# Optimization experiments

Hardware: AMD Instinct MI355X
Metric: run time of the kernel (lower is better)

Reference implementation:

```python
import jax, jax.numpy as jnp
import numpy as np

N_NODES = 50000
N_EDGES = 600000
IN_CH = 128
HID = 128
OUT_CH = 1
N_GRAPHS = 64


def setup_inputs() -> dict:
    key = jax.random.key(0)
    ks = jax.random.split(key, 16)
    inp = {
        "x": jax.random.normal(ks[0], (N_NODES, IN_CH), dtype=jnp.float32),
        "edge_index": jax.random.randint(ks[1], (2, N_EDGES), 0, N_NODES, dtype=jnp.int64),
        "edge_weight": jax.random.uniform(ks[2], (N_EDGES,), dtype=jnp.float32),
        "batch": jnp.sort(jax.random.randint(ks[3], (N_NODES,), 0, N_GRAPHS, dtype=jnp.int64)),
    }
    # SAGEConv params: lin_l (neighbor-aggregate path, has bias) and lin_r (root path)
    dims = [(IN_CH, HID), (HID, HID), (HID, HID), (HID, HID)]
    for i, (din, dout) in enumerate(dims, start=1):
        s = 1.0 / np.sqrt(din)
        inp[f"Wl{i}"] = jax.random.uniform(ks[3 + 2 * i], (din, dout), minval=-s, maxval=s, dtype=jnp.float32)
        inp[f"Wr{i}"] = jax.random.uniform(ks[4 + 2 * i], (din, dout), minval=-s, maxval=s, dtype=jnp.float32)
        inp[f"b{i}"] = jnp.zeros((dout,), dtype=jnp.float32)
    s = 1.0 / np.sqrt(HID)
    inp["Wc"] = jax.random.uniform(ks[14], (HID, OUT_CH), minval=-s, maxval=s, dtype=jnp.float32)
    inp["bc"] = jnp.zeros((OUT_CH,), dtype=jnp.float32)
    return inp


def _sage_conv(x, src, dst, Wl, Wr, b):
    # mean aggregation of source-node features at each destination node
    msg = x[src]  # [E, d] gather
    agg = jax.ops.segment_sum(msg, dst, num_segments=N_NODES)
    cnt = jax.ops.segment_sum(jnp.ones((src.shape[0],), x.dtype), dst, num_segments=N_NODES)
    agg = agg / jnp.maximum(cnt, 1.0)[:, None]
    return agg @ Wl + b + x @ Wr


def reference(x, edge_index, edge_weight, batch,
              Wl1, Wr1, b1, Wl2, Wr2, b2, Wl3, Wr3, b3, Wl4, Wr4, b4, Wc, bc):
    src, dst = edge_index[0], edge_index[1]
    h = jax.nn.relu(_sage_conv(x, src, dst, Wl1, Wr1, b1))
    h = jax.nn.relu(_sage_conv(h, src, dst, Wl2, Wr2, b2))
    h = jax.nn.relu(_sage_conv(h, src, dst, Wl3, Wr3, b3))
    h = jax.nn.relu(_sage_conv(h, src, dst, Wl4, Wr4, b4))
    # global mean pool over graphs
    pooled = jax.ops.segment_sum(h, batch, num_segments=N_GRAPHS)
    gcnt = jax.ops.segment_sum(jnp.ones((N_NODES,), h.dtype), batch, num_segments=N_GRAPHS)
    pooled = pooled / jnp.maximum(gcnt, 1.0)[:, None]  # [G, HID]
    return jax.nn.sigmoid(pooled @ Wc + bc)  # [G, 1]
```

## Files before the change

### kernel.cpp

```cpp
#include <hip/hip_runtime.h>
#include <math.h>

#define NND 50000
#define LNP 50048
#define NED 600000
#define CD  128
#define NG  64
#define NBLK 196
#define GROWS 64

typedef short s8v  __attribute__((ext_vector_type(8)));
typedef float f4v  __attribute__((ext_vector_type(4)));
typedef float f2v  __attribute__((ext_vector_type(2)));
typedef unsigned short u16x4 __attribute__((ext_vector_type(4)));
typedef unsigned short u16x8 __attribute__((ext_vector_type(8)));

static __device__ __forceinline__ unsigned short f2bf(float f) {
  union { float f; unsigned u; } v; v.f = f;
  unsigned r = v.u + 0x7fffu + ((v.u >> 16) & 1u);
  return (unsigned short)(r >> 16);
}
static __device__ __forceinline__ float bf2f(unsigned short h) {
  union { unsigned u; float f; } v; v.u = ((unsigned)h) << 16; return v.f;
}
static __device__ __forceinline__ unsigned f2fp8x4(float a, float b, float c, float d) {
  int r = __builtin_amdgcn_cvt_pk_fp8_f32(a, b, 0, false);
  r = __builtin_amdgcn_cvt_pk_fp8_f32(c, d, r, true);
  return (unsigned)r;
}
static __device__ __forceinline__ void g2lds(const unsigned short* g, unsigned short* l) {
  __builtin_amdgcn_global_load_lds(
      (const __attribute__((address_space(1))) unsigned*)g,
      (__attribute__((address_space(3))) unsigned*)l, 16, 0, 0);
}

__global__ __launch_bounds__(256) void bsum_k(const int* __restrict__ cnt,
                                              int* __restrict__ bsum) {
  __shared__ int s[256];
  int i = blockIdx.x * 256 + threadIdx.x;
  s[threadIdx.x] = (i < NND) ? cnt[i] : 0;
  __syncthreads();
  for (int off = 128; off > 0; off >>= 1) {
    if (threadIdx.x < off) s[threadIdx.x] += s[threadIdx.x + off];
    __syncthreads();
  }
  if (threadIdx.x == 0) bsum[blockIdx.x] = s[0];
}

__global__ __launch_bounds__(256) void bscan_k(const int* __restrict__ bsum,
                                               int* __restrict__ boff,
                                               int* __restrict__ offs,
                                               const int* __restrict__ batch,
                                               int* __restrict__ gb) {
  __shared__ int s[256];
  int t = threadIdx.x;
  if (t <= NG) {
    int lo = 0, hi = NND;
    while (lo < hi) {
      int mid = (lo + hi) >> 1;
      if (batch[mid] < t) lo = mid + 1; else hi = mid;
    }
    gb[t] = lo;
  }
  s[t] = (t < NBLK) ? bsum[t] : 0;
  __syncthreads();
  for (int off = 1; off < 256; off <<= 1) {
    int v = (t >= off) ? s[t - off] : 0;
    __syncthreads();
    s[t] += v;
    __syncthreads();
  }
  if (t < NBLK) boff[t] = (t == 0) ? 0 : s[t - 1];
  if (t == NBLK - 1) offs[NND] = s[t];
}

__global__ __launch_bounds__(256) void escan_k(const int* __restrict__ cnt,
                                               const int* __restrict__ boff,
                                               int* __restrict__ offs,
                                               int* __restrict__ cur) {
  __shared__ int s[256];
  int i = blockIdx.x * 256 + threadIdx.x;
  int t = threadIdx.x;
  int v = (i < NND) ? cnt[i] : 0;
  s[t] = v;
  __syncthreads();
  for (int off = 1; off < 256; off <<= 1) {
    int u = (t >= off) ? s[t - off] : 0;
    __syncthreads();
    s[t] += u;
    __syncthreads();
  }
  if (i < NND) {
    int excl = s[t] - v + boff[blockIdx.x];
    offs[i] = excl;
    cur[i]  = excl;
  }
}

__global__ void fill_k(const int* __restrict__ src, const int* __restrict__ dst,
                       int* __restrict__ cur, int* __restrict__ csr) {
  int e = blockIdx.x * blockDim.x + threadIdx.x;
  if (e >= NED) return;
  int d = dst[e];
  int pos = atomicAdd(&cur[d], 1);
  csr[pos] = src[e];
}

struct WPtrs { const float* w[8]; unsigned short* wt[8]; };
__global__ void prep_k(const float* __restrict__ x, unsigned short* __restrict__ xb,
                       unsigned* __restrict__ x8, WPtrs p,
                       const int* __restrict__ dst, int* __restrict__ cnt) {
  int t = blockIdx.x * blockDim.x + threadIdx.x;
  if (t < NND * 32) {
    float4 v = reinterpret_cast<const float4*>(x)[t];
    u16x4 o;
    o.x = f2bf(v.x); o.y = f2bf(v.y); o.z = f2bf(v.z); o.w = f2bf(v.w);
    reinterpret_cast<u16x4*>(xb)[t] = o;
    x8[t] = f2fp8x4(v.x, v.y, v.z, v.w);
  } else {
    int u = t - NND * 32;
    if (u < 8 * CD * CD) {
      int m = u >> 14, r = u & (CD * CD - 1);
      int n = r >> 7, k = r & 127;
      p.wt[m][r] = f2bf(p.w[m][k * CD + n]);
    } else {
      int e = u - 8 * CD * CD;
      if (e < NED) atomicAdd(&cnt[dst[e]], 1);
    }
  }
}

__global__ __launch_bounds__(256, 4) void sage_k(
    const unsigned* __restrict__ xq, const unsigned short* __restrict__ xb,
    const int* __restrict__ csr, const int* __restrict__ offs,
    const unsigned short* __restrict__ WlT, const unsigned short* __restrict__ WrT,
    const float* __restrict__ bias, unsigned short* __restrict__ hb,
    unsigned char* __restrict__ h8) {
  __shared__ unsigned short abuf[GROWS * CD];
  __shared__ unsigned short xbuf[GROWS * CD];

  const int tid  = threadIdx.x;
  const int wave = tid >> 6;
  const int lane = tid & 63;
  const int quad = lane >> 4;
  const int l16  = lane & 15;
  const size_t rbase = (size_t)blockIdx.x * GROWS;

#pragma unroll
  for (int j = 0; j < 4; ++j) {
    const int s = j * 256 + tid;
    g2lds(xb + (rbase + (s >> 4)) * CD + (s & 15) * 8, &xbuf[(size_t)s * 8]);
  }

  s8v bL[2][4], bR[2][4];
#pragma unroll
  for (int nt = 0; nt < 2; ++nt) {
    const int n = wave * 32 + nt * 16 + l16;
#pragma unroll
    for (int kk = 0; kk < 4; ++kk) {
      size_t woff = (size_t)n * CD + kk * 32 + quad * 8;
      bL[nt][kk] = *reinterpret_cast<const s8v*>(WlT + woff);
      bR[nt][kk] = *reinterpret_cast<const s8v*>(WrT + woff);
    }
  }
  const float bv0 = bias[wave * 32 + l16];
  const float bv1 = bias[wave * 32 + 16 + l16];

  const int team = tid >> 4;
  const int tl   = tid & 15;
  const unsigned* base = xq + tl * 2;
  for (int i = 0; i < 4; ++i) {
    const int rl = team * 4 + i;
    const size_t row = rbase + rl;
    u16x8 o = {};
    if (row < NND) {
      const int e0 = offs[row], e1 = offs[row + 1];
      f2v a01 = {0.f, 0.f}, a23 = {0.f, 0.f}, a45 = {0.f, 0.f}, a67 = {0.f, 0.f};
      int e = e0;
      for (; e + 8 <= e1; e += 8) {
        int s[8];
#pragma unroll
        for (int j = 0; j < 8; ++j) s[j] = csr[e + j];
        uint2 v[8];
#pragma unroll
        for (int j = 0; j < 8; ++j)
          v[j] = *reinterpret_cast<const uint2*>(base + (size_t)s[j] * 32);
#pragma unroll
        for (int j = 0; j < 8; ++j) {
          a01 += __builtin_amdgcn_cvt_pk_f32_fp8(v[j].x, false);
          a23 += __builtin_amdgcn_cvt_pk_f32_fp8(v[j].x, true);
          a45 += __builtin_amdgcn_cvt_pk_f32_fp8(v[j].y, false);
          a67 += __builtin_amdgcn_cvt_pk_f32_fp8(v[j].y, true);
        }
      }
      for (; e + 4 <= e1; e += 4) {
        int s[4];
#pragma unroll
        for (int j = 0; j < 4; ++j) s[j] = csr[e + j];
        uint2 v[4];
#pragma unroll
        for (int j = 0; j < 4; ++j)
          v[j] = *reinterpret_cast<const uint2*>(base + (size_t)s[j] * 32);
#pragma unroll
        for (int j = 0; j < 4; ++j) {
          a01 += __builtin_amdgcn_cvt_pk_f32_fp8(v[j].x, false);
          a23 += __builtin_amdgcn_cvt_pk_f32_fp8(v[j].x, true);
          a45 += __builtin_amdgcn_cvt_pk_f32_fp8(v[j].y, false);
          a67 += __builtin_amdgcn_cvt_pk_f32_fp8(v[j].y, true);
        }
      }
      for (; e < e1; ++e) {
        uint2 v = *reinterpret_cast<const uint2*>(base + (size_t)csr[e] * 32);
        a01 += __builtin_amdgcn_cvt_pk_f32_fp8(v.x, false);
        a23 += __builtin_amdgcn_cvt_pk_f32_fp8(v.x, true);
        a45 += __builtin_amdgcn_cvt_pk_f32_fp8(v.y, false);
        a67 += __builtin_amdgcn_cvt_pk_f32_fp8(v.y, true);
      }
      const float invd = 1.0f / fmaxf((float)(e1 - e0), 1.0f);
      o[0] = f2bf(a01.x * invd); o[1] = f2bf(a01.y * invd);
      o[2] = f2bf(a23.x * invd); o[3] = f2bf(a23.y * invd);
      o[4] = f2bf(a45.x * invd); o[5] = f2bf(a45.y * invd);
      o[6] = f2bf(a67.x * invd); o[7] = f2bf(a67.y * invd);
    }
    *reinterpret_cast<u16x8*>(abuf + rl * CD + tl * 8) = o;
  }

  __syncthreads();

#pragma unroll
  for (int rt = 0; rt < GROWS / 16; ++rt) {
    const unsigned short* arow = abuf + (rt * 16 + l16) * CD + quad * 8;
    const unsigned short* xrow = xbuf + (rt * 16 + l16) * CD + quad * 8;
    f4v acc0 = {}, acc1 = {};
#pragma unroll
    for (int kk = 0; kk < 4; ++kk) {
      s8v aA = *reinterpret_cast<const s8v*>(arow + kk * 32);
      s8v aX = *reinterpret_cast<const s8v*>(xrow + kk * 32);
      acc0 = __builtin_amdgcn_mfma_f32_16x16x32_bf16(aA, bL[0][kk], acc0, 0, 0, 0);
      acc0 = __builtin_amdgcn_mfma_f32_16x16x32_bf16(aX, bR[0][kk], acc0, 0, 0, 0);
      acc1 = __builtin_amdgcn_mfma_f32_16x16x32_bf16(aA, bL[1][kk], acc1, 0, 0, 0);
      acc1 = __builtin_amdgcn_mfma_f32_16x16x32_bf16(aX, bR[1][kk], acc1, 0, 0, 0);
    }
    const size_t row0 = rbase + rt * 16 + quad * 4;
    const int c0 = wave * 32 + l16;
#pragma unroll
    for (int r = 0; r < 4; ++r) {
      const size_t row = row0 + r;
      float v0 = fmaxf(acc0[r] + bv0, 0.0f);
      float v1 = fmaxf(acc1[r] + bv1, 0.0f);
      hb[row * CD + c0]      = f2bf(v0);
      hb[row * CD + c0 + 16] = f2bf(v1);
      if (h8) {
        int p0 = __builtin_amdgcn_cvt_pk_fp8_f32(v0, v0, 0, false);
        int p1 = __builtin_amdgcn_cvt_pk_fp8_f32(v1, v1, 0, false);
        h8[row * CD + c0]      = (unsigned char)p0;
        h8[row * CD + c0 + 16] = (unsigned char)p1;
      }
    }
  }
}

__global__ __launch_bounds__(128) void pool3_k(const unsigned short* __restrict__ h,
                                               const int* __restrict__ batch,
                                               float* __restrict__ pooled) {
  const int c  = threadIdx.x;
  const int r0 = blockIdx.x * 32;
  const int rend = (r0 + 32 < NND) ? r0 + 32 : NND;
  const int g0 = batch[r0];
  const int g1 = batch[rend - 1];
  if (g0 == g1) {
    float acc = 0.f;
#pragma unroll
    for (int i = 0; i < 32; ++i) {
      int row = r0 + i;
      if (row < rend) acc += bf2f(h[(size_t)row * CD + c]);
    }
    atomicAdd(&pooled[g0 * CD + c], acc);
  } else {
    float acc = 0.f;
    int gcur = g0;
    for (int row = r0; row < rend; ++row) {
      int g = batch[row];
      if (g != gcur) {
        atomicAdd(&pooled[gcur * CD + c], acc);
        acc = 0.f; gcur = g;
      }
      acc += bf2f(h[(size_t)row * CD + c]);
    }
    atomicAdd(&pooled[gcur * CD + c], acc);
  }
}

__global__ void final_k(const float* __restrict__ pooled, const int* __restrict__ gb,
                        const float* __restrict__ Wc, const float* __restrict__ bc,
                        float* __restrict__ out) {
  int g = blockIdx.x;
  int lane = threadIdx.x;
  float part = pooled[g * CD + lane] * Wc[lane] +
               pooled[g * CD + 64 + lane] * Wc[64 + lane];
#pragma unroll
  for (int off = 32; off > 0; off >>= 1) part += __shfl_down(part, off, 64);
  if (lane == 0) {
    float cnt = (float)(gb[g + 1] - gb[g]);
    float z = part / fmaxf(cnt, 1.0f) + bc[0];
    out[g] = 1.0f / (1.0f + expf(-z));
  }
}

extern "C" void kernel_launch(void* const* d_in, const int* in_sizes, int n_in,
                              void* d_out, int out_size, void* d_ws, size_t ws_size,
                              hipStream_t stream) {
  const float* x   = (const float*)d_in[0];
  const int*   ei  = (const int*)d_in[1];
  const int*   src = ei;
  const int*   dst = ei + NED;
  const int*   batch = (const int*)d_in[3];
  const float* Wc = (const float*)d_in[16];
  const float* bc = (const float*)d_in[17];
  float* out = (float*)d_out;

  char* w = (char*)d_ws;
  auto alloc = [&](size_t bytes) {
    char* p = w; w += (bytes + 255) & ~(size_t)255; return p;
  };
  int* cnti = (int*)alloc(NND * 4);
  float* pooled = (float*)alloc(NG * CD * 4);
  size_t zspan = (size_t)(w - (char*)cnti);
  int* offs = (int*)alloc((NND + 1) * 4);
  int* cur  = (int*)alloc(NND * 4);
  int* csr  = (int*)alloc((size_t)NED * 4);
  int* gb   = (int*)alloc((NG + 1) * 4);
  int* bsum = (int*)alloc(256 * 4);
  int* boff = (int*)alloc(256 * 4);
  unsigned short* xb0 = (unsigned short*)alloc((size_t)LNP * CD * 2);
  unsigned short* xb1 = (unsigned short*)alloc((size_t)LNP * CD * 2);
  unsigned char* x8a = (unsigned char*)alloc((size_t)LNP * CD);
  unsigned char* x8b = (unsigned char*)alloc((size_t)LNP * CD);
  WPtrs wp;
  for (int i = 0; i < 4; ++i) {
    wp.w[2 * i]     = (const float*)d_in[4 + 3 * i];
    wp.w[2 * i + 1] = (const float*)d_in[5 + 3 * i];
  }
  for (int i = 0; i < 8; ++i) wp.wt[i] = (unsigned short*)alloc(CD * CD * 2);
  const float* bs[4] = {(const float*)d_in[6],  (const float*)d_in[9],
                        (const float*)d_in[12], (const float*)d_in[15]};

  hipMemsetAsync(cnti, 0, zspan, stream);

  prep_k<<<(NND * 32 + 8 * CD * CD + NED + 255) / 256, 256, 0, stream>>>(
      x, xb0, (unsigned*)x8a, wp, dst, cnti);

  bsum_k<<<NBLK, 256, 0, stream>>>(cnti, bsum);
  bscan_k<<<1, 256, 0, stream>>>(bsum, boff, offs, batch, gb);
  escan_k<<<NBLK, 256, 0, stream>>>(cnti, boff, offs, cur);
  fill_k<<<(NED + 255) / 256, 256, 0, stream>>>(src, dst, cur, csr);

  unsigned short* xcur = xb0;
  unsigned short* xnxt = xb1;
  unsigned char* qcur = x8a;
  unsigned char* qnxt = x8b;
  const int ggrid = LNP / GROWS;
  for (int l = 0; l < 4; ++l) {
    sage_k<<<ggrid, 256, 0, stream>>>((const unsigned*)qcur, xcur, csr, offs,
                                      wp.wt[2 * l], wp.wt[2 * l + 1], bs[l],
                                      xnxt, (l < 3) ? qnxt : nullptr);
    unsigned short* t = xcur; xcur = xnxt; xnxt = t;
    unsigned char* q = qcur; qcur = qnxt; qnxt = q;
  }

  pool3_k<<<(NND + 31) / 32, 128, 0, stream>>>(xcur, batch, pooled);
  final_k<<<NG, 64, 0, stream>>>(pooled, gb, Wc, bc, out);
}
```

Before: 327.8 us.

## Fuse global mean pooling into last SAGE layer and widen gather loads

```diff
diff --git a/kernel.cpp b/kernel.cpp
--- a/kernel.cpp
+++ b/kernel.cpp
@@ -135,9 +135,11 @@
     const int* __restrict__ csr, const int* __restrict__ offs,
     const unsigned short* __restrict__ WlT, const unsigned short* __restrict__ WrT,
     const float* __restrict__ bias, unsigned short* __restrict__ hb,
-    unsigned char* __restrict__ h8) {
+    unsigned char* __restrict__ h8, const int* __restrict__ batch,
+    float* __restrict__ pooled) {
   __shared__ unsigned short abuf[GROWS * CD];
   __shared__ unsigned short xbuf[GROWS * CD];
+  __shared__ int sB[GROWS];
 
   const int tid  = threadIdx.x;
   const int wave = tid >> 6;
@@ -152,6 +154,11 @@
     g2lds(xb + (rbase + (s >> 4)) * CD + (s & 15) * 8, &xbuf[(size_t)s * 8]);
   }
 
+  if (pooled && tid < GROWS) {
+    size_t row = rbase + tid;
+    sB[tid] = (row < NND) ? batch[row] : -1;
+  }
+
   s8v bL[2][4], bR[2][4];
 #pragma unroll
   for (int nt = 0; nt < 2; ++nt) {
@@ -166,66 +173,68 @@
   const float bv0 = bias[wave * 32 + l16];
   const float bv1 = bias[wave * 32 + 16 + l16];
 
-  const int team = tid >> 4;
-  const int tl   = tid & 15;
-  const unsigned* base = xq + tl * 2;
-  for (int i = 0; i < 4; ++i) {
-    const int rl = team * 4 + i;
-    const size_t row = rbase + rl;
-    u16x8 o = {};
-    if (row < NND) {
-      const int e0 = offs[row], e1 = offs[row + 1];
-      f2v a01 = {0.f, 0.f}, a23 = {0.f, 0.f}, a45 = {0.f, 0.f}, a67 = {0.f, 0.f};
-      int e = e0;
-      for (; e + 8 <= e1; e += 8) {
-        int s[8];
-#pragma unroll
-        for (int j = 0; j < 8; ++j) s[j] = csr[e + j];
-        uint2 v[8];
-#pragma unroll
-        for (int j = 0; j < 8; ++j)
-          v[j] = *reinterpret_cast<const uint2*>(base + (size_t)s[j] * 32);
-#pragma unroll
-        for (int j = 0; j < 8; ++j) {
-          a01 += __builtin_amdgcn_cvt_pk_f32_fp8(v[j].x, false);
-          a23 += __builtin_amdgcn_cvt_pk_f32_fp8(v[j].x, true);
-          a45 += __builtin_amdgcn_cvt_pk_f32_fp8(v[j].y, false);
-          a67 += __builtin_amdgcn_cvt_pk_f32_fp8(v[j].y, true);
+  {
+    const int team = tid >> 3;
+    const int tl   = tid & 7;
+    const unsigned* base = xq + tl * 4;
+    for (int i = 0; i < 2; ++i) {
+      const int rl = team * 2 + i;
+      const size_t row = rbase + rl;
+      u16x8 o0 = {}, o1 = {};
+      if (row < NND) {
+        const int e0 = offs[row], e1 = offs[row + 1];
+        f2v a[8] = {};
+        int e = e0;
+        for (; e + 4 <= e1; e += 4) {
+          int s[4];
+#pragma unroll
+          for (int j = 0; j < 4; ++j) s[j] = csr[e + j];
+          uint4 v[4];
+#pragma unroll
+          for (int j = 0; j < 4; ++j)
+            v[j] = *reinterpret_cast<const uint4*>(base + (size_t)s[j] * 32);
+#pragma unroll
+          for (int j = 0; j < 4; ++j) {
+            a[0] += __builtin_amdgcn_cvt_pk_f32_fp8(v[j].x, false);
+            a[1] += __builtin_amdgcn_cvt_pk_f32_fp8(v[j].x, true);
+            a[2] += __builtin_amdgcn_cvt_pk_f32_fp8(v[j].y, false);
+            a[3] += __builtin_amdgcn_cvt_pk_f32_fp8(v[j].y, true);
+            a[4] += __builtin_amdgcn_cvt_pk_f32_fp8(v[j].z, false);
+            a[5] += __builtin_amdgcn_cvt_pk_f32_fp8(v[j].z, true);
+            a[6] += __builtin_amdgcn_cvt_pk_f32_fp8(v[j].w, false);
+            a[7] += __builtin_amdgcn_cvt_pk_f32_fp8(v[j].w, true);
+          }
+        }
+        for (; e < e1; ++e) {
+          uint4 v = *reinterpret_cast<const uint4*>(base + (size_t)csr[e] * 32);
+          a[0] += __builtin_amdgcn_cvt_pk_f32_fp8(v.x, false);
+          a[1] += __builtin_amdgcn_cvt_pk_f32_fp8(v.x, true);
+          a[2] += __builtin_amdgcn_cvt_pk_f32_fp8(v.y, false);
+          a[3] += __builtin_amdgcn_cvt_pk_f32_fp8(v.y, true);
+          a[4] += __builtin_amdgcn_cvt_pk_f32_fp8(v.z, false);
+          a[5] += __builtin_amdgcn_cvt_pk_f32_fp8(v.z, true);
+          a[6] += __builtin_amdgcn_cvt_pk_f32_fp8(v.w, false);
+          a[7] += __builtin_amdgcn_cvt_pk_f32_fp8(v.w, true);
+        }
+        const float invd = 1.0f / fmaxf((float)(e1 - e0), 1.0f);
+#pragma unroll
+        for (int c = 0; c < 4; ++c) {
+          o0[2 * c]     = f2bf(a[c].x * invd);
+          o0[2 * c + 1] = f2bf(a[c].y * invd);
+          o1[2 * c]     = f2bf(a[4 + c].x * invd);
+          o1[2 * c + 1] = f2bf(a[4 + c].y * invd);
         }
       }
-      for (; e + 4 <= e1; e += 4) {
-        int s[4];
-#pragma unroll
-        for (int j = 0; j < 4; ++j) s[j] = csr[e + j];
-        uint2 v[4];
-#pragma unroll
-        for (int j = 0; j < 4; ++j)
-          v[j] = *reinterpret_cast<const uint2*>(base + (size_t)s[j] * 32);
-#pragma unroll
-        for (int j = 0; j < 4; ++j) {
-          a01 += __builtin_amdgcn_cvt_pk_f32_fp8(v[j].x, false);
-          a23 += __builtin_amdgcn_cvt_pk_f32_fp8(v[j].x, true);
-          a45 += __builtin_amdgcn_cvt_pk_f32_fp8(v[j].y, false);
-          a67 += __builtin_amdgcn_cvt_pk_f32_fp8(v[j].y, true);
-        }
-      }
-      for (; e < e1; ++e) {
-        uint2 v = *reinterpret_cast<const uint2*>(base + (size_t)csr[e] * 32);
-        a01 += __builtin_amdgcn_cvt_pk_f32_fp8(v.x, false);
-        a23 += __builtin_amdgcn_cvt_pk_f32_fp8(v.x, true);
-        a45 += __builtin_amdgcn_cvt_pk_f32_fp8(v.y, false);
-        a67 += __builtin_amdgcn_cvt_pk_f32_fp8(v.y, true);
-      }
-      const float invd = 1.0f / fmaxf((float)(e1 - e0), 1.0f);
-      o[0] = f2bf(a01.x * invd); o[1] = f2bf(a01.y * invd);
-      o[2] = f2bf(a23.x * invd); o[3] = f2bf(a23.y * invd);
-      o[4] = f2bf(a45.x * invd); o[5] = f2bf(a45.y * invd);
-      o[6] = f2bf(a67.x * invd); o[7] = f2bf(a67.y * invd);
-    }
-    *reinterpret_cast<u16x8*>(abuf + rl * CD + tl * 8) = o;
+      *reinterpret_cast<u16x8*>(abuf + rl * CD + tl * 16)     = o0;
+      *reinterpret_cast<u16x8*>(abuf + rl * CD + tl * 16 + 8) = o1;
+    }
   }
 
   __syncthreads();
+
+  const bool fast = pooled && (rbase + GROWS <= NND) && (sB[0] == sB[GROWS - 1]);
+  const int c0 = wave * 32 + l16;
+  float p0 = 0.f, p1 = 0.f;
 
 #pragma unroll
   for (int rt = 0; rt < GROWS / 16; ++rt) {
@@ -242,52 +251,45 @@
       acc1 = __builtin_amdgcn_mfma_f32_16x16x32_bf16(aX, bR[1][kk], acc1, 0, 0, 0);
     }
     const size_t row0 = rbase + rt * 16 + quad * 4;
-    const int c0 = wave * 32 + l16;
 #pragma unroll
     for (int r = 0; r < 4; ++r) {
       const size_t row = row0 + r;
       float v0 = fmaxf(acc0[r] + bv0, 0.0f);
       float v1 = fmaxf(acc1[r] + bv1, 0.0f);
-      hb[row * CD + c0]      = f2bf(v0);
-      hb[row * CD + c0 + 16] = f2bf(v1);
+      if (hb) {
+        hb[row * CD + c0]      = f2bf(v0);
+        hb[row * CD + c0 + 16] = f2bf(v1);
+      }
       if (h8) {
-        int p0 = __builtin_amdgcn_cvt_pk_fp8_f32(v0, v0, 0, false);
-        int p1 = __builtin_amdgcn_cvt_pk_fp8_f32(v1, v1, 0, false);
-        h8[row * CD + c0]      = (unsigned char)p0;
-        h8[row * CD + c0 + 16] = (unsigned char)p1;
+        int q0 = __builtin_amdgcn_cvt_pk_fp8_f32(v0, v0, 0, false);
+        int q1 = __builtin_amdgcn_cvt_pk_fp8_f32(v1, v1, 0, false);
+        h8[row * CD + c0]      = (unsigned char)q0;
+        h8[row * CD + c0 + 16] = (unsigned char)q1;
       }
-    }
-  }
-}
-
-__global__ __launch_bounds__(128) void pool3_k(const unsigned short* __restrict__ h,
-                                               const int* __restrict__ batch,
-                                               float* __restrict__ pooled) {
-  const int c  = threadIdx.x;
-  const int r0 = blockIdx.x * 32;
-  const int rend = (r0 + 32 < NND) ? r0 + 32 : NND;
-  const int g0 = batch[r0];
-  const int g1 = batch[rend - 1];
-  if (g0 == g1) {
-    float acc = 0.f;
-#pragma unroll
-    for (int i = 0; i < 32; ++i) {
-      int row = r0 + i;
-      if (row < rend) acc += bf2f(h[(size_t)row * CD + c]);
-    }
-    atomicAdd(&pooled[g0 * CD + c], acc);
-  } else {
-    float acc = 0.f;
-    int gcur = g0;
-    for (int row = r0; row < rend; ++row) {
-      int g = batch[row];
-      if (g != gcur) {
-        atomicAdd(&pooled[gcur * CD + c], acc);
-        acc = 0.f; gcur = g;
+      if (pooled) {
+        if (fast) {
+          p0 += v0; p1 += v1;
+        } else {
+          int g = sB[rt * 16 + quad * 4 + r];
+          if (g >= 0) {
+            atomicAdd(&pooled[g * CD + c0], v0);
+            atomicAdd(&pooled[g * CD + c0 + 16], v1);
+          }
+        }
       }
-      acc += bf2f(h[(size_t)row * CD + c]);
-    }
-    atomicAdd(&pooled[gcur * CD + c], acc);
+    }
+  }
+
+  if (fast) {
+    p0 += __shfl_xor(p0, 16, 64);
+    p0 += __shfl_xor(p0, 32, 64);
+    p1 += __shfl_xor(p1, 16, 64);
+    p1 += __shfl_xor(p1, 32, 64);
+    if (quad == 0) {
+      const int g = sB[0];
+      atomicAdd(&pooled[g * CD + c0], p0);
+      atomicAdd(&pooled[g * CD + c0 + 16], p1);
+    }
   }
 }
 
@@ -361,13 +363,18 @@
   unsigned char* qnxt = x8b;
   const int ggrid = LNP / GROWS;
   for (int l = 0; l < 4; ++l) {
-    sage_k<<<ggrid, 256, 0, stream>>>((const unsigned*)qcur, xcur, csr, offs,
-                                      wp.wt[2 * l], wp.wt[2 * l + 1], bs[l],
-                                      xnxt, (l < 3) ? qnxt : nullptr);
-    unsigned short* t = xcur; xcur = xnxt; xnxt = t;
-    unsigned char* q = qcur; qcur = qnxt; qnxt = q;
-  }
-
-  pool3_k<<<(NND + 31) / 32, 128, 0, stream>>>(xcur, batch, pooled);
+    if (l < 3) {
+      sage_k<<<ggrid, 256, 0, stream>>>((const unsigned*)qcur, xcur, csr, offs,
+                                        wp.wt[2 * l], wp.wt[2 * l + 1], bs[l],
+                                        xnxt, qnxt, batch, nullptr);
+      unsigned short* t = xcur; xcur = xnxt; xnxt = t;
+      unsigned char* q = qcur; qcur = qnxt; qnxt = q;
+    } else {
+      sage_k<<<ggrid, 256, 0, stream>>>((const unsigned*)qcur, xcur, csr, offs,
+                                        wp.wt[2 * l], wp.wt[2 * l + 1], bs[l],
+                                        nullptr, nullptr, batch, pooled);
+    }
+  }
+
   final_k<<<NG, 64, 0, stream>>>(pooled, gb, Wc, bc, out);
 }
```

Measured after the change: 308.2 us. 6.0% less time.
